# Kernel tuning notes

Hardware: AMD Instinct MI355X
Metric: run time of the kernel (lower is better)

The kernel has to match this reference:

```python
import jax, jax.numpy as jnp
import numpy as np

B, T, Z, AE, H, M, A = 32, 512, 128, 16, 1024, 5, 18
OUT = Z * 3 * M + 1  # 1921
K = M * Z  # per-component split size for logmix/mu/logstd


def setup_inputs() -> dict:
    key = jax.random.key(0)
    ks = jax.random.split(key, 9)
    s = 0.02
    return {
        "z": jax.random.normal(ks[0], (B, T, Z), jnp.float32),
        "actions": jax.random.randint(ks[1], (B, T), 0, A, jnp.int32),
        "dones": jax.random.randint(ks[2], (B, T), 0, 2, jnp.int32),
        "embed": jax.random.normal(ks[3], (A, AE), jnp.float32) * s,
        "W_ih": jax.random.normal(ks[4], (4 * H, Z + AE), jnp.float32) * s,
        "W_hh": jax.random.normal(ks[5], (4 * H, H), jnp.float32) * s,
        "b_ih": jnp.zeros((4 * H,), jnp.float32),
        "b_hh": jnp.zeros((4 * H,), jnp.float32),
        "W_out": jax.random.normal(ks[6], (OUT, H), jnp.float32) * s,
        "b_out": jnp.zeros((OUT,), jnp.float32),
    }


def reference(z, actions, dones, embed, W_ih, W_hh, b_ih, b_hh, W_out, b_out):
    a_emb = embed[actions]                              # [B,T,AE]
    inp = jnp.concatenate([z, a_emb], axis=2)           # [B,T,Z+AE]
    d = dones.astype(inp.dtype)                         # [B,T]
    # precompute input contribution to gates for all timesteps (one big GEMM)
    x_pre = jnp.einsum('btf,gf->btg', inp, W_ih) + b_ih + b_hh  # [B,T,4H]

    def cell(carry, xt):
        h, c = carry
        xg, dt = xt                                     # xg: [B,4H], dt: [B]
        gates = xg + h @ W_hh.T
        i, f, g, o = jnp.split(gates, 4, axis=1)        # torch LSTMCell order i,f,g,o
        c_new = jax.nn.sigmoid(f) * c + jax.nn.sigmoid(i) * jnp.tanh(g)
        h_new = jax.nn.sigmoid(o) * jnp.tanh(c_new)
        mask = (1.0 - dt)[:, None]                      # done-masking AFTER output
        return (h_new * mask, c_new * mask), h_new

    h0 = jnp.zeros((B, H), inp.dtype)
    _, hs = jax.lax.scan(cell, (h0, h0), (x_pre.transpose(1, 0, 2), d.T))
    hs = hs.transpose(1, 0, 2)[:, :-1]                  # [B,T-1,H]
    out = hs @ W_out.T + b_out                          # [B,T-1,OUT]

    logmix = out[..., :K].reshape(-1, M)
    mu = out[..., K:2 * K].reshape(-1, M)
    logstd = out[..., 2 * K:3 * K].reshape(-1, M)
    done_p = out[..., 3 * K:].squeeze(-1)               # [B,T-1]
    logmix = logmix - jax.scipy.special.logsumexp(logmix, axis=1, keepdims=True)
    return logmix, mu, logstd, done_p
```

## Files before the change

kernel.cpp:

```cpp
#include <hip/hip_runtime.h>
#include <hip/hip_bf16.h>


typedef float f4 __attribute__((ext_vector_type(4)));
typedef short s8 __attribute__((ext_vector_type(8)));
typedef unsigned short us8v __attribute__((ext_vector_type(8)));
typedef unsigned short us4v __attribute__((ext_vector_type(4)));
typedef unsigned long long u64;
typedef unsigned u32;

#define DEV __device__ __forceinline__

DEV unsigned short f2b(float f) {
  unsigned u = __float_as_uint(f);
  return (unsigned short)((u + 0x7FFFu + ((u >> 16) & 1u)) >> 16);
}
DEV float b2f(unsigned short s) { return __uint_as_float(((unsigned)s) << 16); }

DEV f4 MFMA(s8 a, s8 b, f4 c) {
  return __builtin_amdgcn_mfma_f32_16x16x32_bf16(a, b, c, 0, 0, 0);
}
DEV s8 LD8(const unsigned short* p) { return *reinterpret_cast<const s8*>(p); }

DEV u32 AL32(const u32* p) {
  return __hip_atomic_load(p, __ATOMIC_RELAXED, __HIP_MEMORY_SCOPE_AGENT);
}
DEV void AS(u64* p, u64 v) {
  __hip_atomic_store(p, v, __ATOMIC_RELAXED, __HIP_MEMORY_SCOPE_AGENT);
}

DEV float sigf(float x) {
  float e = __builtin_amdgcn_exp2f(x * -1.44269504f);
  return __builtin_amdgcn_rcpf(1.f + e);
}
DEV float tanhf_fast(float x) {
  float e = __builtin_amdgcn_exp2f(x * 2.88539008f);
  return 1.f - 2.f * __builtin_amdgcn_rcpf(e + 1.f);
}

static constexpr size_t WS_GCNT = 0;
static constexpr size_t WS_NACT = 2048;
static constexpr size_t WS_HDR  = 4096;
static constexpr size_t WS_META = 4352;
static constexpr size_t WS_LOFF = 69888;
static constexpr size_t WS_TMP  = 131072;
static constexpr size_t WS_ZT   = 131072;
static constexpr size_t WS_WOUT = 4325376;
static constexpr size_t WS_HS2  = 8261632;
static constexpr size_t WS_END  = 41816064;
static constexpr size_t DO_CALL = 35651584;

__global__ void cvt_wout_k(const float* __restrict__ W, unsigned short* __restrict__ o) {
  int i = blockIdx.x * 256 + threadIdx.x;
  if (i < 491776) {
    const float4 v = reinterpret_cast<const float4*>(W)[i];
    us4v u; u[0] = f2b(v.x); u[1] = f2b(v.y); u[2] = f2b(v.z); u[3] = f2b(v.w);
    reinterpret_cast<us4v*>(o)[i] = u;
  }
}

__global__ void cvt_z_k(const float* __restrict__ z, unsigned short* __restrict__ zt) {
  int i = blockIdx.x * 256 + threadIdx.x;
  if (i < 524288) {
    const float4 v = reinterpret_cast<const float4*>(z)[i];
    us4v u; u[0] = f2b(v.x); u[1] = f2b(v.y); u[2] = f2b(v.z); u[3] = f2b(v.w);
    reinterpret_cast<us4v*>(zt)[i] = u;
  }
}

__global__ void zero_hs_tail_k(u64* __restrict__ hs2) {
  int i = blockIdx.x * 256 + threadIdx.x;
  if (i < 8192) {
    int region = i >> 6, rr = (i & 63) >> 1, hf = i & 1;
    hs2[((size_t)region * 16384 + 16352 + rr) * 2 + hf] = 0ull;
  }
}

__global__ __launch_bounds__(256) void seg_build_k(
    const int* __restrict__ dones, u32* __restrict__ tmp,
    u32* __restrict__ meta, u32* __restrict__ nact, u32* __restrict__ hdr,
    u32* __restrict__ loff) {
  __shared__ u32 hist[512];
  __shared__ u32 cur[512];
  __shared__ u32 scnt[32];
  const int tid = threadIdx.x;
  for (int i = tid; i < 512; i += 256) hist[i] = 0;
  __syncthreads();
  if (tid < 32) {
    int b = tid, cnt = 0, t0 = 0;
    for (int t = 1; t <= 511; ++t) {
      bool brk = (t == 511) || (dones[b * 512 + t - 1] != 0);
      if (brk) {
        int len = t - t0;
        tmp[b * 511 + cnt] = ((u32)t0 << 16) | (u32)len;
        atomicAdd(&hist[len], 1u);
        ++cnt; t0 = t;
      }
    }
    scnt[b] = (u32)cnt;
  }
  __syncthreads();
  if (tid == 0) {
    u32 acc = 0; int ml = 0;
    for (int L = 511; L >= 0; --L) {
      cur[L] = acc; nact[L] = acc;
      if (hist[L] && !ml) ml = L;
      acc += hist[L];
    }
    hdr[0] = acc; hdr[1] = (u32)ml;
    u32 off = 0; loff[0] = 0;
    for (int s2 = 1; s2 <= ml; ++s2) { loff[s2] = off; off += nact[s2]; }
  }
  __syncthreads();
  if (tid < 32) {
    int b = tid; u32 c = scnt[b];
    for (u32 i = 0; i < c; ++i) {
      u32 e = tmp[b * 511 + i];
      u32 len = e & 0xFFFFu, t0 = e >> 16;
      u32 slot = atomicAdd(&cur[len], 1u);
      meta[slot] = ((u32)b << 20) | (t0 << 10) | len;
    }
  }
}

__global__ __launch_bounds__(512, 1) void lstm_seg_k(
    const float* __restrict__ Whh, const float* __restrict__ Wih,
    const float* __restrict__ embed, const float* __restrict__ bih,
    const float* __restrict__ bhh, const int* __restrict__ actions,
    const unsigned short* __restrict__ zt, const u32* __restrict__ meta,
    const u32* __restrict__ nact, const u32* __restrict__ hdr,
    const u32* __restrict__ loff, u64* __restrict__ hsl,
    u64* __restrict__ c_all, u64* __restrict__ hs2,
    u32* __restrict__ gcnt) {
  const int blk = blockIdx.x;
  const int g = blk >> 1;
  const int half = blk & 1;
  const int tid = threadIdx.x;
  const int lane = tid & 63;
  const int w = tid >> 6;
  const int ln = lane & 15, lk = lane >> 4;

  __shared__ alignas(16) unsigned short whh_sw[32 * 2 * 64 * 8];
  __shared__ alignas(16) unsigned short wz_sw[4 * 2 * 64 * 8];
  __shared__ float abias[18][32];
  __shared__ float red[8][64][33];

  for (int i = tid; i < 32768; i += 512) {
    int j = i & 7, L = (i >> 3) & 63, nt = (i >> 9) & 1, kt = i >> 10;
    int n = nt * 16 + (L & 15);
    int grow = (n >> 3) * 1024 + g * 8 + (n & 7);
    int k = kt * 32 + ((L >> 4) << 3) + j;
    whh_sw[i] = f2b(Whh[grow * 1024 + k]);
  }
  for (int i = tid; i < 4096; i += 512) {
    int j = i & 7, L = (i >> 3) & 63, nt = (i >> 9) & 1, kz = i >> 10;
    int n = nt * 16 + (L & 15);
    int grow = (n >> 3) * 1024 + g * 8 + (n & 7);
    int k = kz * 32 + ((L >> 4) << 3) + j;
    wz_sw[i] = f2b(Wih[grow * 144 + k]);
  }
  for (int i = tid; i < 18 * 32; i += 512) {
    int a = i >> 5, n = i & 31;
    int grow = (n >> 3) * 1024 + g * 8 + (n & 7);
    float s = bih[grow] + bhh[grow];
    for (int j = 0; j < 16; ++j) s += embed[a * 16 + j] * Wih[grow * 144 + 128 + j];
    abias[a][n] = s;
  }
  __syncthreads();

  const int maxlen = (int)hdr[1];

  for (int s = 0; s < maxlen; ++s) {
    const u32 N = nact[s];
    const int ntiles = (int)((N + 63) >> 6);
    const u64* hread = hsl + (size_t)loff[s] * 256;
    u64* hwrite = hsl + (size_t)loff[s + 1] * 256;

    for (int tile = half + 2 * w; tile < ntiles; tile += 16) {
      const u32 sb = (u32)tile << 6;
      const u32 slot = sb + (u32)lane;
      const bool valid = slot < N;
      const u32 m = valid ? meta[slot] : 0u;
      const u32 b = m >> 20, t0 = (m >> 10) & 1023u, L = m & 1023u;
      const int zrow = (int)(b * 512u + t0 + (u32)s);
      const int orow = (int)(b * 511u + t0 + (u32)s);
      const u32 act = valid ? (u32)actions[zrow] : 0u;
      u64 cq[4] = {0, 0, 0, 0};
      if (s && valid) {
        const u64* cp = c_all + ((size_t)blk << 15) + ((size_t)slot << 2);
        cq[0] = cp[0]; cq[1] = cp[1]; cq[2] = cp[2]; cq[3] = cp[3];
      }
      int zr[4];
#pragma unroll
      for (int q = 0; q < 4; ++q) zr[q] = __shfl(zrow, ln + 16 * q, 64);

      f4 a00 = {0,0,0,0}, a01 = {0,0,0,0}, a10 = {0,0,0,0}, a11 = {0,0,0,0};
      f4 a20 = {0,0,0,0}, a21 = {0,0,0,0}, a30 = {0,0,0,0}, a31 = {0,0,0,0};
#pragma unroll
      for (int kz = 0; kz < 4; ++kz) {
        s8 b0 = LD8(wz_sw + (((kz * 2 + 0) * 64 + lane) << 3));
        s8 b1 = LD8(wz_sw + (((kz * 2 + 1) * 64 + lane) << 3));
        s8 f0 = LD8(zt + (size_t)zr[0] * 128 + kz * 32 + (lk << 3));
        s8 f1 = LD8(zt + (size_t)zr[1] * 128 + kz * 32 + (lk << 3));
        s8 f2 = LD8(zt + (size_t)zr[2] * 128 + kz * 32 + (lk << 3));
        s8 f3 = LD8(zt + (size_t)zr[3] * 128 + kz * 32 + (lk << 3));
        a00 = MFMA(f0, b0, a00);  a01 = MFMA(f0, b1, a01);
        a10 = MFMA(f1, b0, a10);  a11 = MFMA(f1, b1, a11);
        a20 = MFMA(f2, b0, a20);  a21 = MFMA(f2, b1, a21);
        a30 = MFMA(f3, b0, a30);  a31 = MFMA(f3, b1, a31);
      }
      if (s) {
        const u32 r0c = (sb + (u32)ln      < N) ? sb + (u32)ln      : N - 1u;
        const u32 r1c = (sb + (u32)ln + 16 < N) ? sb + (u32)ln + 16 : N - 1u;
        const u32 r2c = (sb + (u32)ln + 32 < N) ? sb + (u32)ln + 32 : N - 1u;
        const u32 r3c = (sb + (u32)ln + 48 < N) ? sb + (u32)ln + 48 : N - 1u;
        const unsigned short* h0 =
            (const unsigned short*)(hread + (size_t)r0c * 256) + (lk << 3);
        const unsigned short* h1 =
            (const unsigned short*)(hread + (size_t)r1c * 256) + (lk << 3);
        const unsigned short* h2 =
            (const unsigned short*)(hread + (size_t)r2c * 256) + (lk << 3);
        const unsigned short* h3 =
            (const unsigned short*)(hread + (size_t)r3c * 256) + (lk << 3);
#pragma unroll 8
        for (int kt = 0; kt < 32; ++kt) {
          s8 b0 = LD8(whh_sw + (((kt * 2 + 0) * 64 + lane) << 3));
          s8 b1 = LD8(whh_sw + (((kt * 2 + 1) * 64 + lane) << 3));
          s8 f0 = LD8(h0 + (kt << 5));
          s8 f1 = LD8(h1 + (kt << 5));
          s8 f2 = LD8(h2 + (kt << 5));
          s8 f3 = LD8(h3 + (kt << 5));
          a00 = MFMA(f0, b0, a00);  a01 = MFMA(f0, b1, a01);
          a10 = MFMA(f1, b0, a10);  a11 = MFMA(f1, b1, a11);
          a20 = MFMA(f2, b0, a20);  a21 = MFMA(f2, b1, a21);
          a30 = MFMA(f3, b0, a30);  a31 = MFMA(f3, b1, a31);
        }
      }

#pragma unroll
      for (int j = 0; j < 4; ++j) {
        red[w][(lk << 2) + j][ln]           = a00[j];
        red[w][(lk << 2) + j][16 + ln]      = a01[j];
        red[w][16 + (lk << 2) + j][ln]      = a10[j];
        red[w][16 + (lk << 2) + j][16 + ln] = a11[j];
        red[w][32 + (lk << 2) + j][ln]      = a20[j];
        red[w][32 + (lk << 2) + j][16 + ln] = a21[j];
        red[w][48 + (lk << 2) + j][ln]      = a30[j];
        red[w][48 + (lk << 2) + j][16 + ln] = a31[j];
      }
      const bool carry = valid && (L > (u32)(s + 1));
      u32 cb[8]; unsigned short hb[8];
#pragma unroll
      for (int e = 0; e < 8; ++e) {
        float gi = red[w][lane][e]      + abias[act][e];
        float gf = red[w][lane][8 + e]  + abias[act][8 + e];
        float gg = red[w][lane][16 + e] + abias[act][16 + e];
        float go = red[w][lane][24 + e] + abias[act][24 + e];
        const u32 cpb = (e & 1) ? (u32)(cq[e >> 1] >> 32) : (u32)cq[e >> 1];
        const float cprev = __uint_as_float(cpb);
        const float si = sigf(gi), sf = sigf(gf), so = sigf(go);
        const float cn = sf * cprev + si * tanhf_fast(gg);
        const float hn = so * tanhf_fast(cn);
        cb[e] = __float_as_uint(cn);
        hb[e] = f2b(hn);
      }
      if (carry) {
        u64* cp = c_all + ((size_t)blk << 15) + ((size_t)slot << 2);
        cp[0] = ((u64)cb[1] << 32) | (u64)cb[0];
        cp[1] = ((u64)cb[3] << 32) | (u64)cb[2];
        cp[2] = ((u64)cb[5] << 32) | (u64)cb[4];
        cp[3] = ((u64)cb[7] << 32) | (u64)cb[6];
      }
      const u64 hu0 = (u64)hb[0] | ((u64)hb[1] << 16) |
                      ((u64)hb[2] << 32) | ((u64)hb[3] << 48);
      const u64 hu1 = (u64)hb[4] | ((u64)hb[5] << 16) |
                      ((u64)hb[6] << 32) | ((u64)hb[7] << 48);
      if (valid) {
        u64* hp = hs2 + ((size_t)g * 16384 + orow) * 2;
        hp[0] = hu0; hp[1] = hu1;
        if (carry) {
          AS(hwrite + (size_t)slot * 256 + 2 * g, hu0);
          AS(hwrite + (size_t)slot * 256 + 2 * g + 1, hu1);
        }
      }
    }

    asm volatile("s_waitcnt vmcnt(0)" ::: "memory");
    __syncthreads();
    if (s + 1 < maxlen) {
      if (tid == 0) {
        __hip_atomic_fetch_add(gcnt + (blk >> 4) * 32, 1u,
                               __ATOMIC_RELAXED, __HIP_MEMORY_SCOPE_AGENT);
        const u32 tgt = (u32)(s + 1) * 16u;
        for (u32 spin = 0; spin < (1u << 20); ++spin) {
          u32 mn = 0xFFFFFFFFu;
#pragma unroll
          for (int gg2 = 0; gg2 < 16; ++gg2) {
            u32 v = AL32(gcnt + gg2 * 32);
            mn = (v < mn) ? v : mn;
          }
          if (mn >= tgt) break;
          __builtin_amdgcn_s_sleep(1);
        }
      }
      __syncthreads();
    }
  }
}

__global__ __launch_bounds__(256, 2) void out_gemm_k(
    const u64* __restrict__ hs2, const unsigned short* __restrict__ wout,
    const float* __restrict__ b_out, float* __restrict__ out) {
  const int mblk = blockIdx.x, nblk = blockIdx.y;
  const int tid = threadIdx.x, lane = tid & 63, w = tid >> 6;
  const int ln = lane & 15, lk = lane >> 4;
  __shared__ alignas(16) unsigned char smraw[43520];
  unsigned short* bsm = (unsigned short*)smraw;
  float* ep = (float*)smraw;
  const bool last = (nblk == 23);

  if (last) {
    for (int i = tid; i < 15 * 136; i += 256) bsm[81 * 136 + i] = 0;
  }
  __syncthreads();

  const int r0 = mblk * 128 + w * 16;
  f4 accA[5], accB[5];
#pragma unroll
  for (int s = 0; s < 5; ++s) {
    accA[s] = (f4){0.f, 0.f, 0.f, 0.f};
    accB[s] = (f4){0.f, 0.f, 0.f, 0.f};
  }
  f4 acc5A = {0.f, 0.f, 0.f, 0.f}, acc5B = {0.f, 0.f, 0.f, 0.f};

  for (int kc = 0; kc < 8; ++kc) {
#pragma unroll
    for (int ii = 0; ii < 5; ++ii) {
      int i = tid + ii * 256;
      int n = i >> 4, k16 = i & 15;
      us8v v = *reinterpret_cast<const us8v*>(
          wout + (size_t)(nblk * 80 + n) * 1024 + kc * 128 + (k16 << 3));
      *reinterpret_cast<us8v*>(bsm + n * 136 + (k16 << 3)) = v;
    }
    if (last && tid < 16) {
      us8v v = *reinterpret_cast<const us8v*>(
          wout + (size_t)1920 * 1024 + kc * 128 + (tid << 3));
      *reinterpret_cast<us8v*>(bsm + 80 * 136 + (tid << 3)) = v;
    }
    __syncthreads();
#pragma unroll
    for (int ks = 0; ks < 4; ++ks) {
      const int k0 = kc * 128 + ks * 32 + (lk << 3);
      s8 aLo = *reinterpret_cast<const s8*>(
          hs2 + ((size_t)(k0 >> 3) * 16384 + r0 + ln) * 2);
      s8 aHi = *reinterpret_cast<const s8*>(
          hs2 + ((size_t)(k0 >> 3) * 16384 + r0 + 64 + ln) * 2);
#pragma unroll
      for (int s = 0; s < 5; ++s) {
        s8 b = LD8(bsm + (s * 16 + ln) * 136 + ks * 32 + (lk << 3));
        accA[s] = MFMA(aLo, b, accA[s]);
        accB[s] = MFMA(aHi, b, accB[s]);
      }
      if (last) {
        s8 b6 = LD8(bsm + ((80 + ln) * 136) + ks * 32 + (lk << 3));
        acc5A = MFMA(aLo, b6, acc5A);
        acc5B = MFMA(aHi, b6, acc5B);
      }
    }
    __syncthreads();
  }

  const int T = nblk >> 3;
  if (T) {
    float* base = out + (size_t)10465280 * T;
    const int lc0 = (nblk - (T << 3)) * 80;
#pragma unroll
    for (int s = 0; s < 5; ++s) {
      const int lc = lc0 + s * 16 + ln;
      const float bias = b_out[T * 640 + lc];
#pragma unroll
      for (int j = 0; j < 4; ++j) {
        const int rowA = r0 + (lk << 2) + j;
        const int rowB = rowA + 64;
        if (rowA < 16352) base[(size_t)rowA * 640 + lc] = accA[s][j] + bias;
        if (rowB < 16352) base[(size_t)rowB * 640 + lc] = accB[s][j] + bias;
      }
    }
    if (last && ln == 0) {
      const float bias = b_out[1920];
#pragma unroll
      for (int j = 0; j < 4; ++j) {
        const int rowA = r0 + (lk << 2) + j;
        const int rowB = rowA + 64;
        if (rowA < 16352) out[31395840 + rowA] = acc5A[j] + bias;
        if (rowB < 16352) out[31395840 + rowB] = acc5B[j] + bias;
      }
    }
  } else {
#pragma unroll
    for (int s = 0; s < 5; ++s) {
      const float bias = b_out[nblk * 80 + s * 16 + ln];
#pragma unroll
      for (int j = 0; j < 4; ++j) {
        ep[(w * 16 + (lk << 2) + j) * 84 + s * 16 + ln]        = accA[s][j] + bias;
        ep[(64 + w * 16 + (lk << 2) + j) * 84 + s * 16 + ln]   = accB[s][j] + bias;
      }
    }
    __syncthreads();
    for (int task = tid; task < 2048; task += 256) {
      const int rr = task >> 4, grp = task & 15;
      const int row = mblk * 128 + rr;
      const float* e = ep + rr * 84 + grp * 5;
      float v0 = e[0], v1 = e[1], v2 = e[2], v3 = e[3], v4 = e[4];
      float mx = fmaxf(fmaxf(fmaxf(v0, v1), fmaxf(v2, v3)), v4);
      float ssum = expf(v0 - mx) + expf(v1 - mx) + expf(v2 - mx) +
                   expf(v3 - mx) + expf(v4 - mx);
      float lse = mx + logf(ssum);
      if (row < 16352) {
        float* o = out + (size_t)row * 640 + nblk * 80 + grp * 5;
        o[0] = v0 - lse; o[1] = v1 - lse; o[2] = v2 - lse;
        o[3] = v3 - lse; o[4] = v4 - lse;
      }
    }
  }
}

extern "C" void kernel_launch(void* const* d_in, const int* in_sizes, int n_in,
                              void* d_out, int out_size, void* d_ws, size_t ws_size,
                              hipStream_t stream) {
  const float* z       = (const float*)d_in[0];
  const int*   actions = (const int*)d_in[1];
  const int*   dones   = (const int*)d_in[2];
  const float* embed   = (const float*)d_in[3];
  const float* Wih     = (const float*)d_in[4];
  const float* Whh     = (const float*)d_in[5];
  const float* bih     = (const float*)d_in[6];
  const float* bhh     = (const float*)d_in[7];
  const float* Wout    = (const float*)d_in[8];
  const float* bout    = (const float*)d_in[9];
  float* out = (float*)d_out;

  if (ws_size < WS_END) return;

  char* ws = (char*)d_ws;
  u32* gcnt              = (u32*)(ws + WS_GCNT);
  u32* nact              = (u32*)(ws + WS_NACT);
  u32* hdr               = (u32*)(ws + WS_HDR);
  u32* metaA             = (u32*)(ws + WS_META);
  u32* loff              = (u32*)(ws + WS_LOFF);
  u32* tmp               = (u32*)(ws + WS_TMP);
  unsigned short* zt     = (unsigned short*)(ws + WS_ZT);
  unsigned short* wout16 = (unsigned short*)(ws + WS_WOUT);
  u64* hs2               = (u64*)(ws + WS_HS2);
  u64* hsl   = (u64*)d_out;
  u64* call  = (u64*)((char*)d_out + DO_CALL);

  hipMemsetAsync(d_ws, 0, 2048, stream);

  seg_build_k<<<1, 256, 0, stream>>>(dones, tmp, metaA, nact, hdr, loff);
  cvt_z_k<<<2048, 256, 0, stream>>>(z, zt);
  zero_hs_tail_k<<<32, 256, 0, stream>>>(hs2);
  lstm_seg_k<<<256, 512, 0, stream>>>(Whh, Wih, embed, bih, bhh, actions,
                                      zt, metaA, nact, hdr, loff, hsl, call,
                                      hs2, gcnt);
  cvt_wout_k<<<1921, 256, 0, stream>>>(Wout, wout16);
  out_gemm_k<<<dim3(128, 24), 256, 0, stream>>>(hs2, wout16, bout, out);
}
```

Baseline: 856.3 us.

## Merge prep kernels and widen output GEMM N-tile to 160 columns

New measurement: 870.5 us. About the same (+1.7%).

```diff
diff --git a/kernel.cpp b/kernel.cpp
--- a/kernel.cpp
+++ b/kernel.cpp
@@ -50,29 +50,29 @@
 static constexpr size_t WS_END  = 41816064;
 static constexpr size_t DO_CALL = 35651584;
 
-__global__ void cvt_wout_k(const float* __restrict__ W, unsigned short* __restrict__ o) {
-  int i = blockIdx.x * 256 + threadIdx.x;
-  if (i < 491776) {
-    const float4 v = reinterpret_cast<const float4*>(W)[i];
-    us4v u; u[0] = f2b(v.x); u[1] = f2b(v.y); u[2] = f2b(v.z); u[3] = f2b(v.w);
-    reinterpret_cast<us4v*>(o)[i] = u;
-  }
-}
-
-__global__ void cvt_z_k(const float* __restrict__ z, unsigned short* __restrict__ zt) {
-  int i = blockIdx.x * 256 + threadIdx.x;
-  if (i < 524288) {
+__global__ void prep_k(const float* __restrict__ z, unsigned short* __restrict__ zt,
+                       const float* __restrict__ W, unsigned short* __restrict__ wout16,
+                       u64* __restrict__ hs2) {
+  const int bid = blockIdx.x;
+  const int tid = threadIdx.x;
+  if (bid < 2048) {
+    int i = bid * 256 + tid;
     const float4 v = reinterpret_cast<const float4*>(z)[i];
     us4v u; u[0] = f2b(v.x); u[1] = f2b(v.y); u[2] = f2b(v.z); u[3] = f2b(v.w);
     reinterpret_cast<us4v*>(zt)[i] = u;
-  }
-}
-
-__global__ void zero_hs_tail_k(u64* __restrict__ hs2) {
-  int i = blockIdx.x * 256 + threadIdx.x;
-  if (i < 8192) {
-    int region = i >> 6, rr = (i & 63) >> 1, hf = i & 1;
-    hs2[((size_t)region * 16384 + 16352 + rr) * 2 + hf] = 0ull;
+  } else if (bid < 3970) {
+    int i = (bid - 2048) * 256 + tid;
+    if (i < 491776) {
+      const float4 v = reinterpret_cast<const float4*>(W)[i];
+      us4v u; u[0] = f2b(v.x); u[1] = f2b(v.y); u[2] = f2b(v.z); u[3] = f2b(v.w);
+      reinterpret_cast<us4v*>(wout16)[i] = u;
+    }
+  } else {
+    int i = (bid - 3970) * 256 + tid;
+    if (i < 8192) {
+      int region = i >> 6, rr = (i & 63) >> 1, hf = i & 1;
+      hs2[((size_t)region * 16384 + 16352 + rr) * 2 + hf] = 0ull;
+    }
   }
 }
 
@@ -314,20 +314,20 @@
   const int mblk = blockIdx.x, nblk = blockIdx.y;
   const int tid = threadIdx.x, lane = tid & 63, w = tid >> 6;
   const int ln = lane & 15, lk = lane >> 4;
-  __shared__ alignas(16) unsigned char smraw[43520];
+  __shared__ alignas(16) unsigned char smraw[47872];
   unsigned short* bsm = (unsigned short*)smraw;
   float* ep = (float*)smraw;
-  const bool last = (nblk == 23);
+  const bool last = (nblk == 11);
 
   if (last) {
-    for (int i = tid; i < 15 * 136; i += 256) bsm[81 * 136 + i] = 0;
+    for (int i = tid; i < 15 * 136; i += 256) bsm[161 * 136 + i] = 0;
   }
   __syncthreads();
 
   const int r0 = mblk * 128 + w * 16;
-  f4 accA[5], accB[5];
-#pragma unroll
-  for (int s = 0; s < 5; ++s) {
+  f4 accA[10], accB[10];
+#pragma unroll
+  for (int s = 0; s < 10; ++s) {
     accA[s] = (f4){0.f, 0.f, 0.f, 0.f};
     accB[s] = (f4){0.f, 0.f, 0.f, 0.f};
   }
@@ -335,17 +335,17 @@
 
   for (int kc = 0; kc < 8; ++kc) {
 #pragma unroll
-    for (int ii = 0; ii < 5; ++ii) {
+    for (int ii = 0; ii < 10; ++ii) {
       int i = tid + ii * 256;
       int n = i >> 4, k16 = i & 15;
       us8v v = *reinterpret_cast<const us8v*>(
-          wout + (size_t)(nblk * 80 + n) * 1024 + kc * 128 + (k16 << 3));
+          wout + (size_t)(nblk * 160 + n) * 1024 + kc * 128 + (k16 << 3));
       *reinterpret_cast<us8v*>(bsm + n * 136 + (k16 << 3)) = v;
     }
     if (last && tid < 16) {
       us8v v = *reinterpret_cast<const us8v*>(
           wout + (size_t)1920 * 1024 + kc * 128 + (tid << 3));
-      *reinterpret_cast<us8v*>(bsm + 80 * 136 + (tid << 3)) = v;
+      *reinterpret_cast<us8v*>(bsm + 160 * 136 + (tid << 3)) = v;
     }
     __syncthreads();
 #pragma unroll
@@ -356,13 +356,13 @@
       s8 aHi = *reinterpret_cast<const s8*>(
           hs2 + ((size_t)(k0 >> 3) * 16384 + r0 + 64 + ln) * 2);
 #pragma unroll
-      for (int s = 0; s < 5; ++s) {
+      for (int s = 0; s < 10; ++s) {
         s8 b = LD8(bsm + (s * 16 + ln) * 136 + ks * 32 + (lk << 3));
         accA[s] = MFMA(aLo, b, accA[s]);
         accB[s] = MFMA(aHi, b, accB[s]);
       }
       if (last) {
-        s8 b6 = LD8(bsm + ((80 + ln) * 136) + ks * 32 + (lk << 3));
+        s8 b6 = LD8(bsm + ((160 + ln) * 136) + ks * 32 + (lk << 3));
         acc5A = MFMA(aLo, b6, acc5A);
         acc5B = MFMA(aHi, b6, acc5B);
       }
@@ -370,12 +370,12 @@
     __syncthreads();
   }
 
-  const int T = nblk >> 3;
+  const int T = nblk >> 2;
   if (T) {
     float* base = out + (size_t)10465280 * T;
-    const int lc0 = (nblk - (T << 3)) * 80;
-#pragma unroll
-    for (int s = 0; s < 5; ++s) {
+    const int lc0 = (nblk & 3) * 160;
+#pragma unroll
+    for (int s = 0; s < 10; ++s) {
       const int lc = lc0 + s * 16 + ln;
       const float bias = b_out[T * 640 + lc];
 #pragma unroll
@@ -398,28 +398,33 @@
     }
   } else {
 #pragma unroll
-    for (int s = 0; s < 5; ++s) {
-      const float bias = b_out[nblk * 80 + s * 16 + ln];
-#pragma unroll
-      for (int j = 0; j < 4; ++j) {
-        ep[(w * 16 + (lk << 2) + j) * 84 + s * 16 + ln]        = accA[s][j] + bias;
-        ep[(64 + w * 16 + (lk << 2) + j) * 84 + s * 16 + ln]   = accB[s][j] + bias;
-      }
-    }
-    __syncthreads();
-    for (int task = tid; task < 2048; task += 256) {
-      const int rr = task >> 4, grp = task & 15;
-      const int row = mblk * 128 + rr;
-      const float* e = ep + rr * 84 + grp * 5;
-      float v0 = e[0], v1 = e[1], v2 = e[2], v3 = e[3], v4 = e[4];
-      float mx = fmaxf(fmaxf(fmaxf(v0, v1), fmaxf(v2, v3)), v4);
-      float ssum = expf(v0 - mx) + expf(v1 - mx) + expf(v2 - mx) +
-                   expf(v3 - mx) + expf(v4 - mx);
-      float lse = mx + logf(ssum);
-      if (row < 16352) {
-        float* o = out + (size_t)row * 640 + nblk * 80 + grp * 5;
-        o[0] = v0 - lse; o[1] = v1 - lse; o[2] = v2 - lse;
-        o[3] = v3 - lse; o[4] = v4 - lse;
+    for (int ph = 0; ph < 2; ++ph) {
+      __syncthreads();
+#pragma unroll
+      for (int sl = 0; sl < 5; ++sl) {
+        const int s = ph * 5 + sl;
+        const float bias = b_out[nblk * 160 + s * 16 + ln];
+#pragma unroll
+        for (int j = 0; j < 4; ++j) {
+          ep[(w * 16 + (lk << 2) + j) * 84 + sl * 16 + ln]      = accA[s][j] + bias;
+          ep[(64 + w * 16 + (lk << 2) + j) * 84 + sl * 16 + ln] = accB[s][j] + bias;
+        }
+      }
+      __syncthreads();
+      for (int task = tid; task < 2048; task += 256) {
+        const int rr = task >> 4, grp = task & 15;
+        const int row = mblk * 128 + rr;
+        const float* e = ep + rr * 84 + grp * 5;
+        float v0 = e[0], v1 = e[1], v2 = e[2], v3 = e[3], v4 = e[4];
+        float mx = fmaxf(fmaxf(fmaxf(v0, v1), fmaxf(v2, v3)), v4);
+        float ssum = expf(v0 - mx) + expf(v1 - mx) + expf(v2 - mx) +
+                     expf(v3 - mx) + expf(v4 - mx);
+        float lse = mx + logf(ssum);
+        if (row < 16352) {
+          float* o = out + (size_t)row * 640 + nblk * 160 + ph * 80 + grp * 5;
+          o[0] = v0 - lse; o[1] = v1 - lse; o[2] = v2 - lse;
+          o[3] = v3 - lse; o[4] = v4 - lse;
+        }
       }
     }
   }
@@ -458,11 +463,9 @@
   hipMemsetAsync(d_ws, 0, 2048, stream);
 
   seg_build_k<<<1, 256, 0, stream>>>(dones, tmp, metaA, nact, hdr, loff);
-  cvt_z_k<<<2048, 256, 0, stream>>>(z, zt);
-  zero_hs_tail_k<<<32, 256, 0, stream>>>(hs2);
+  prep_k<<<4002, 256, 0, stream>>>(z, zt, Wout, wout16, hs2);
   lstm_seg_k<<<256, 512, 0, stream>>>(Whh, Wih, embed, bih, bhh, actions,
                                       zt, metaA, nact, hdr, loff, hsl, call,
                                       hs2, gcnt);
-  cvt_wout_k<<<1921, 256, 0, stream>>>(Wout, wout16);
-  out_gemm_k<<<dim3(128, 24), 256, 0, stream>>>(hs2, wout16, bout, out);
-}
+  out_gemm_k<<<dim3(128, 12), 256, 0, stream>>>(hs2, wout16, bout, out);
+}
```
